# Performance work log

Hardware: AMD Instinct MI355X
Metric: run time of the kernel (lower is better)

Reference implementation:

```python
import jax, jax.numpy as jnp
import numpy as np

B, S, D, H, FF = 2, 1024, 1024, 16, 4096
EPS = 1e-6  # flax LayerNorm default


def _layernorm(x, scale, bias):
    m = jnp.mean(x, axis=-1, keepdims=True)
    v = jnp.mean(jnp.square(x - m), axis=-1, keepdims=True)
    return (x - m) * jax.lax.rsqrt(v + EPS) * scale + bias


def _attention(x, mask, w_qkv, b_qkv, w_o, b_o):
    # projection to 3*D, split into q,k,v
    p = x @ w_qkv + b_qkv                       # (B,S,3D)
    q, k, v = jnp.split(p, 3, axis=-1)          # each (B,S,D)
    hd = D // H
    # NOTE: faithful to source -- heads formed by a plain reshape of (B,S,D)
    qh = q.reshape(B, H, S, hd)
    kh = k.reshape(B, H, S, hd)
    vh = v.reshape(B, H, S, hd)
    # NOTE: scaled by sqrt(full hidden dim D), as in source (dim_key = key.shape[-1])
    scores = jnp.einsum('bhqd,bhkd->bhqk', qh, kh) / jnp.sqrt(jnp.asarray(D, x.dtype))
    scores = scores * mask                      # multiplicative mask (faithful)
    attn = jax.nn.softmax(scores, axis=-1)      # (B,H,S,S)
    ctx = jnp.einsum('bhqk,bhkd->bhqd', attn, vh).reshape(B, S, D)
    return ctx @ w_o + b_o, attn


def _geglu_ffn(x, w1, b1, wg, bg, w2, b2):
    h = x @ w1 + b1                              # (B,S,FF)
    g = h @ wg + bg                              # (B,S,2*FF)
    a, gate = g[..., :FF], g[..., FF:]
    tanh_res = jnp.tanh(gate * 0.7978845608 * (1 + 0.044715 * gate ** 2))
    act = a * 0.5 * gate * (1 + tanh_res)
    return act @ w2 + b2


def setup_inputs() -> dict:
    key = jax.random.key(0)
    ks = jax.random.split(key, 16)
    sc = 0.02
    inp = {
        'x': jax.random.normal(ks[0], (B, S, D), jnp.float32),
        'ln1_s': jnp.ones((D,), jnp.float32), 'ln1_b': jnp.zeros((D,), jnp.float32),
        'w_qkv1': jax.random.normal(ks[1], (D, 3 * D), jnp.float32) * sc,
        'b_qkv1': jnp.zeros((3 * D,), jnp.float32),
        'w_o1': jax.random.normal(ks[2], (D, D), jnp.float32) * sc,
        'b_o1': jnp.zeros((D,), jnp.float32),
        'ln2_s': jnp.ones((D,), jnp.float32), 'ln2_b': jnp.zeros((D,), jnp.float32),
        'w_qkv2': jax.random.normal(ks[3], (D, 3 * D), jnp.float32) * sc,
        'b_qkv2': jnp.zeros((3 * D,), jnp.float32),
        'w_o2': jax.random.normal(ks[4], (D, D), jnp.float32) * sc,
        'b_o2': jnp.zeros((D,), jnp.float32),
        'ln3_s': jnp.ones((D,), jnp.float32), 'ln3_b': jnp.zeros((D,), jnp.float32),
        'w1': jax.random.normal(ks[5], (D, FF), jnp.float32) * sc,
        'b1': jnp.zeros((FF,), jnp.float32),
        'wg': jax.random.normal(ks[6], (FF, 2 * FF), jnp.float32) * sc,
        'bg': jnp.zeros((2 * FF,), jnp.float32),
        'w2': jax.random.normal(ks[7], (FF, D), jnp.float32) * sc,
        'b2': jnp.zeros((D,), jnp.float32),
    }
    return inp


def reference(x, ln1_s, ln1_b, w_qkv1, b_qkv1, w_o1, b_o1,
              ln2_s, ln2_b, w_qkv2, b_qkv2, w_o2, b_o2,
              ln3_s, ln3_b, w1, b1, wg, bg, w2, b2):
    # causal mask: lower-triangular ones, multiplicative, broadcast over (B,H)
    mask = (jnp.arange(S)[:, None] >= jnp.arange(S)[None, :]).astype(jnp.int32)
    mask = jnp.broadcast_to(mask[None, None], (B, H, S, S))

    x = _layernorm(x, ln1_s, ln1_b)
    att1, attn_w1 = _attention(x, mask, w_qkv1, b_qkv1, w_o1, b_o1)
    x = x + att1                                  # dropout deterministic (identity)
    x = _layernorm(x, ln2_s, ln2_b)
    att2, attn_w2 = _attention(x, mask, w_qkv2, b_qkv2, w_o2, b_o2)
    x = x + att2
    x = _layernorm(x, ln3_s, ln3_b)
    out = _geglu_ffn(x, w1, b1, wg, bg, w2, b2)
    # NOTE: faithful to source -- final residual adds attention2 output
    x = out + att2
    return (x, attn_w1, attn_w2)
```

## Files before the change

kernel.cpp:

```cpp
#include <hip/hip_runtime.h>
#include <hip/hip_bf16.h>

#define B_ 2
#define S_ 1024
#define D_ 1024
#define H_ 16
#define HD_ 64
#define FF_ 4096
#define NROW_ (B_*S_)

typedef __hip_bfloat16 bf16;
typedef float f32x4 __attribute__((ext_vector_type(4)));
typedef int int4v __attribute__((ext_vector_type(4)));
typedef __bf16 bf16x8 __attribute__((ext_vector_type(8)));

__device__ __forceinline__ float bf2f(unsigned short u){
  return __uint_as_float((unsigned)u << 16);
}
__device__ __forceinline__ unsigned short f2bf(float f){
  unsigned u = __float_as_uint(f);
  return (unsigned short)((u + 0x7FFFu + ((u >> 16) & 1u)) >> 16);
}
__device__ __forceinline__ float gelu_gate(float a, float g){
  float t = tanhf(0.7978845608f * g * (1.f + 0.044715f * g * g));
  return a * 0.5f * g * (1.f + t);
}


__global__ __launch_bounds__(256) void tcvt(const float* __restrict__ W,
    unsigned short* __restrict__ Wt, int K, int N){
  __shared__ float tile[32][33];
  const int k0 = blockIdx.y*32, n0 = blockIdx.x*32;
  const int t = threadIdx.x;
  #pragma unroll
  for (int i = 0; i < 4; i++){
    int idx = t + i*256; int r = idx>>5, c = idx&31;
    tile[r][c] = W[(size_t)(k0+r)*N + n0 + c];
  }
  __syncthreads();
  #pragma unroll
  for (int i = 0; i < 4; i++){
    int idx = t + i*256; int r = idx>>5, c = idx&31;
    Wt[(size_t)(n0+r)*K + k0 + c] = f2bf(tile[c][r]);
  }
}

__global__ __launch_bounds__(256) void lnb_k(const float* __restrict__ x,
    const float* __restrict__ sc, const float* __restrict__ bi, unsigned short* __restrict__ y){
  const int row = blockIdx.x;
  const int t = threadIdx.x;
  const float* xr = x + (size_t)row * D_;
  float4 v = *(const float4*)&xr[t*4];
  __shared__ float red[8];
  float sum = v.x + v.y + v.z + v.w;
  #pragma unroll
  for (int o = 32; o > 0; o >>= 1) sum += __shfl_down(sum, o);
  if ((t & 63) == 0) red[t >> 6] = sum;
  __syncthreads();
  if (t == 0) red[4] = (red[0]+red[1]+red[2]+red[3]) * (1.f / D_);
  __syncthreads();
  const float mean = red[4];
  const float dx = v.x-mean, dy = v.y-mean, dz = v.z-mean, dw = v.w-mean;
  float sq = dx*dx + dy*dy + dz*dz + dw*dw;
  #pragma unroll
  for (int o = 32; o > 0; o >>= 1) sq += __shfl_down(sq, o);
  if ((t & 63) == 0) red[t >> 6] = sq;
  __syncthreads();
  if (t == 0) red[5] = (red[0]+red[1]+red[2]+red[3]) * (1.f / D_);
  __syncthreads();
  const float rstd = rsqrtf(red[5] + 1e-6f);
  float4 s4 = *(const float4*)&sc[t*4];
  float4 b4 = *(const float4*)&bi[t*4];
  ushort4 ov;
  ov.x = f2bf(dx*rstd*s4.x + b4.x);
  ov.y = f2bf(dy*rstd*s4.y + b4.y);
  ov.z = f2bf(dz*rstd*s4.z + b4.z);
  ov.w = f2bf(dw*rstd*s4.w + b4.w);
  *(ushort4*)&y[(size_t)row*D_ + t*4] = ov;
}

template<bool HAS_RES, bool RES_BF16, bool OUT_BF16>
__global__ __launch_bounds__(256) void mgemm(const unsigned short* __restrict__ A,
    const unsigned short* __restrict__ Bt, const float* __restrict__ bias,
    const void* __restrict__ res, void* __restrict__ Cv, int M, int N, int K){
  __shared__ unsigned short As[128*32];
  __shared__ unsigned short Bs[128*32];
  const int tid = threadIdx.x;
  const int bm = blockIdx.y*128, bn = blockIdx.x*128;
  const int lane = tid & 63, lq = lane >> 4, lr = lane & 15;
  const int wv = tid >> 6, wr = wv >> 1, wc = wv & 1;
  f32x4 acc[4][4] = {};
  int4v ra[2], rb[2];
  #pragma unroll
  for (int i = 0; i < 2; i++){
    int f = tid + i*256; int row = f>>2, s = f&3;
    ra[i] = *(const int4v*)&A[(size_t)(bm+row)*K + s*8];
    rb[i] = *(const int4v*)&Bt[(size_t)(bn+row)*K + s*8];
  }
  for (int k0 = 0; k0 < K; k0 += 32){
    __syncthreads();
    #pragma unroll
    for (int i = 0; i < 2; i++){
      int f = tid + i*256; int row = f>>2, s = f&3;
      int off = row*32 + ((s + (row>>1))&3)*8;
      *(int4v*)&As[off] = ra[i];
      *(int4v*)&Bs[off] = rb[i];
    }
    __syncthreads();
    if (k0 + 32 < K){
      #pragma unroll
      for (int i = 0; i < 2; i++){
        int f = tid + i*256; int row = f>>2, s = f&3;
        ra[i] = *(const int4v*)&A[(size_t)(bm+row)*K + k0+32 + s*8];
        rb[i] = *(const int4v*)&Bt[(size_t)(bn+row)*K + k0+32 + s*8];
      }
    }
    bf16x8 af[4], bfr[4];
    #pragma unroll
    for (int fm = 0; fm < 4; fm++){
      int r = wr*64 + fm*16 + lr;
      af[fm] = *(const bf16x8*)&As[r*32 + ((lq + (r>>1))&3)*8];
    }
    #pragma unroll
    for (int fn = 0; fn < 4; fn++){
      int r = wc*64 + fn*16 + lr;
      bfr[fn] = *(const bf16x8*)&Bs[r*32 + ((lq + (r>>1))&3)*8];
    }
    #pragma unroll
    for (int fm = 0; fm < 4; fm++)
      #pragma unroll
      for (int fn = 0; fn < 4; fn++)
        acc[fm][fn] = __builtin_amdgcn_mfma_f32_16x16x32_bf16(af[fm], bfr[fn], acc[fm][fn], 0, 0, 0);
  }
  #pragma unroll
  for (int fm = 0; fm < 4; fm++)
    #pragma unroll
    for (int fn = 0; fn < 4; fn++)
      #pragma unroll
      for (int rr = 0; rr < 4; rr++){
        int r = bm + wr*64 + fm*16 + lq*4 + rr;
        int c = bn + wc*64 + fn*16 + lr;
        size_t o = (size_t)r*N + c;
        float v = acc[fm][fn][rr] + bias[c];
        if (HAS_RES){
          if (RES_BF16) v += bf2f(((const unsigned short*)res)[o]);
          else          v += ((const float*)res)[o];
        }
        if (OUT_BF16) ((unsigned short*)Cv)[o] = f2bf(v);
        else          ((float*)Cv)[o] = v;
      }
}

__global__ __launch_bounds__(256) void mqkv(const unsigned short* __restrict__ A,
    const unsigned short* __restrict__ Bt, const float* __restrict__ bias,
    unsigned short* __restrict__ qh, unsigned short* __restrict__ kh, unsigned short* __restrict__ vt){
  const int K = D_;
  __shared__ unsigned short As[128*32];
  __shared__ unsigned short Bs[128*32];
  const int tid = threadIdx.x;
  const int bm = blockIdx.y*128, bn = blockIdx.x*128;
  const int lane = tid & 63, lq = lane >> 4, lr = lane & 15;
  const int wv = tid >> 6, wr = wv >> 1, wc = wv & 1;
  f32x4 acc[4][4] = {};
  int4v ra[2], rb[2];
  #pragma unroll
  for (int i = 0; i < 2; i++){
    int f = tid + i*256; int row = f>>2, s = f&3;
    ra[i] = *(const int4v*)&A[(size_t)(bm+row)*K + s*8];
    rb[i] = *(const int4v*)&Bt[(size_t)(bn+row)*K + s*8];
  }
  for (int k0 = 0; k0 < K; k0 += 32){
    __syncthreads();
    #pragma unroll
    for (int i = 0; i < 2; i++){
      int f = tid + i*256; int row = f>>2, s = f&3;
      int off = row*32 + ((s + (row>>1))&3)*8;
      *(int4v*)&As[off] = ra[i];
      *(int4v*)&Bs[off] = rb[i];
    }
    __syncthreads();
    if (k0 + 32 < K){
      #pragma unroll
      for (int i = 0; i < 2; i++){
        int f = tid + i*256; int row = f>>2, s = f&3;
        ra[i] = *(const int4v*)&A[(size_t)(bm+row)*K + k0+32 + s*8];
        rb[i] = *(const int4v*)&Bt[(size_t)(bn+row)*K + k0+32 + s*8];
      }
    }
    bf16x8 af[4], bfr[4];
    #pragma unroll
    for (int fm = 0; fm < 4; fm++){
      int r = wr*64 + fm*16 + lr;
      af[fm] = *(const bf16x8*)&As[r*32 + ((lq + (r>>1))&3)*8];
    }
    #pragma unroll
    for (int fn = 0; fn < 4; fn++){
      int r = wc*64 + fn*16 + lr;
      bfr[fn] = *(const bf16x8*)&Bs[r*32 + ((lq + (r>>1))&3)*8];
    }
    #pragma unroll
    for (int fm = 0; fm < 4; fm++)
      #pragma unroll
      for (int fn = 0; fn < 4; fn++)
        acc[fm][fn] = __builtin_amdgcn_mfma_f32_16x16x32_bf16(af[fm], bfr[fn], acc[fm][fn], 0, 0, 0);
  }
  #pragma unroll
  for (int fm = 0; fm < 4; fm++)
    #pragma unroll
    for (int fn = 0; fn < 4; fn++){
      int cbase = bn + wc*64 + fn*16 + lr;
      float bv = bias[cbase];
      if (cbase < 2*D_){
        unsigned short* dst = (cbase < D_) ? qh : kh;
        int cc = cbase & (D_-1);
        int u = cc >> 6, d2 = cc & 63;
        #pragma unroll
        for (int rr = 0; rr < 4; rr++){
          int r = bm + wr*64 + fm*16 + lq*4 + rr;
          int b = r >> 10, s = r & (S_-1);
          int h = s >> 6;
          int s2 = ((s & 63) << 4) + u;
          size_t off = (((size_t)(b*H_ + h))*S_ + s2)*HD_ + d2;
          dst[off] = f2bf(acc[fm][fn][rr] + bv);
        }
      } else {
        int cc = cbase - 2*D_;
        int u = cc >> 6, d2 = cc & 63;
        #pragma unroll
        for (int rr = 0; rr < 4; rr++){
          int r = bm + wr*64 + fm*16 + lq*4 + rr;
          int b = r >> 10, s = r & (S_-1);
          int h = s >> 6;
          int s2 = ((s & 63) << 4) + u;
          size_t off = (((size_t)(b*H_ + h))*HD_ + d2)*S_ + s2;
          vt[off] = f2bf(acc[fm][fn][rr] + bv);
        }
      }
    }
}

__global__ __launch_bounds__(256) void mgeglu(const unsigned short* __restrict__ A,
    const unsigned short* __restrict__ Wt, const float* __restrict__ bgp, unsigned short* __restrict__ act){
  const int K = FF_;
  __shared__ unsigned short As[128*32];
  __shared__ unsigned short Ba[64*32];
  __shared__ unsigned short Bg[64*32];
  const int tid = threadIdx.x;
  const int bm = blockIdx.y*128, bn = blockIdx.x*64;
  const int lane = tid & 63, lq = lane >> 4, lr = lane & 15;
  const int wv = tid >> 6, wr = wv >> 1, wc = wv & 1;
  f32x4 aa[4][2] = {};
  f32x4 ag[4][2] = {};
  int4v ra[2], rba, rbg;
  #pragma unroll
  for (int i = 0; i < 2; i++){
    int f = tid + i*256; int row = f>>2, s = f&3;
    ra[i] = *(const int4v*)&A[(size_t)(bm+row)*K + s*8];
  }
  { int row = tid>>2, s = tid&3;
    rba = *(const int4v*)&Wt[(size_t)(bn+row)*K + s*8];
    rbg = *(const int4v*)&Wt[(size_t)(FF_+bn+row)*K + s*8];
  }
  for (int k0 = 0; k0 < K; k0 += 32){
    __syncthreads();
    #pragma unroll
    for (int i = 0; i < 2; i++){
      int f = tid + i*256; int row = f>>2, s = f&3;
      *(int4v*)&As[row*32 + ((s + (row>>1))&3)*8] = ra[i];
    }
    { int row = tid>>2, s = tid&3;
      int off = row*32 + ((s + (row>>1))&3)*8;
      *(int4v*)&Ba[off] = rba;
      *(int4v*)&Bg[off] = rbg;
    }
    __syncthreads();
    if (k0 + 32 < K){
      #pragma unroll
      for (int i = 0; i < 2; i++){
        int f = tid + i*256; int row = f>>2, s = f&3;
        ra[i] = *(const int4v*)&A[(size_t)(bm+row)*K + k0+32 + s*8];
      }
      { int row = tid>>2, s = tid&3;
        rba = *(const int4v*)&Wt[(size_t)(bn+row)*K + k0+32 + s*8];
        rbg = *(const int4v*)&Wt[(size_t)(FF_+bn+row)*K + k0+32 + s*8];
      }
    }
    bf16x8 af[4], fa[2], fg[2];
    #pragma unroll
    for (int fm = 0; fm < 4; fm++){
      int r = wr*64 + fm*16 + lr;
      af[fm] = *(const bf16x8*)&As[r*32 + ((lq + (r>>1))&3)*8];
    }
    #pragma unroll
    for (int fn = 0; fn < 2; fn++){
      int r = wc*32 + fn*16 + lr;
      int off = r*32 + ((lq + (r>>1))&3)*8;
      fa[fn] = *(const bf16x8*)&Ba[off];
      fg[fn] = *(const bf16x8*)&Bg[off];
    }
    #pragma unroll
    for (int fm = 0; fm < 4; fm++)
      #pragma unroll
      for (int fn = 0; fn < 2; fn++){
        aa[fm][fn] = __builtin_amdgcn_mfma_f32_16x16x32_bf16(af[fm], fa[fn], aa[fm][fn], 0, 0, 0);
        ag[fm][fn] = __builtin_amdgcn_mfma_f32_16x16x32_bf16(af[fm], fg[fn], ag[fm][fn], 0, 0, 0);
      }
  }
  #pragma unroll
  for (int fm = 0; fm < 4; fm++)
    #pragma unroll
    for (int fn = 0; fn < 2; fn++)
      #pragma unroll
      for (int rr = 0; rr < 4; rr++){
        int r = bm + wr*64 + fm*16 + lq*4 + rr;
        int c = bn + wc*32 + fn*16 + lr;
        float a = aa[fm][fn][rr] + bgp[c];
        float g = ag[fm][fn][rr] + bgp[FF_ + c];
        act[(size_t)r*FF_ + c] = f2bf(gelu_gate(a, g));
      }
}

__global__ __launch_bounds__(256) void mscore(const unsigned short* __restrict__ qh,
    const unsigned short* __restrict__ kh, float* __restrict__ attn){
  const int kt = blockIdx.x, qt = blockIdx.y, bh = blockIdx.z;
  const int tid = threadIdx.x;
  const int lane = tid & 63, lq = lane >> 4, lr = lane & 15;
  const int wv = tid >> 6, wr = wv >> 1, wc = wv & 1;
  float* Ap = attn + (((size_t)bh*S_ + qt*128))*S_ + kt*128;

  if (kt > qt){
    #pragma unroll
    for (int i = 0; i < 16; i++){
      int f = tid + i*256;
      int r = f >> 5, c4 = f & 31;
      float4 z = {0.f,0.f,0.f,0.f};
      *(float4*)&Ap[(size_t)r*S_ + c4*4] = z;
    }
    return;
  }

  __shared__ unsigned short Qs[128*64];
  __shared__ unsigned short Ks[128*64];
  const unsigned short* Qp = qh + ((size_t)bh*S_ + qt*128)*HD_;
  const unsigned short* Kp = kh + ((size_t)bh*S_ + kt*128)*HD_;
  #pragma unroll
  for (int i = 0; i < 4; i++){
    int f = tid + i*256;
    int row = f >> 3, s = f & 7;
    int off = row*64 + ((s + row)&7)*8;
    *(int4v*)&Qs[off] = *(const int4v*)&Qp[(size_t)row*HD_ + s*8];
    *(int4v*)&Ks[off] = *(const int4v*)&Kp[(size_t)row*HD_ + s*8];
  }
  __syncthreads();
  f32x4 acc[4][4] = {};
  #pragma unroll
  for (int ks = 0; ks < 2; ks++){
    bf16x8 af[4], bfr[4];
    #pragma unroll
    for (int fm = 0; fm < 4; fm++){
      int r = wr*64 + fm*16 + lr;
      int j = ks*4 + lq;
      af[fm] = *(const bf16x8*)&Qs[r*64 + ((j + r)&7)*8];
    }
    #pragma unroll
    for (int fn = 0; fn < 4; fn++){
      int r = wc*64 + fn*16 + lr;
      int j = ks*4 + lq;
      bfr[fn] = *(const bf16x8*)&Ks[r*64 + ((j + r)&7)*8];
    }
    #pragma unroll
    for (int fm = 0; fm < 4; fm++)
      #pragma unroll
      for (int fn = 0; fn < 4; fn++)
        acc[fm][fn] = __builtin_amdgcn_mfma_f32_16x16x32_bf16(af[fm], bfr[fn], acc[fm][fn], 0, 0, 0);
  }
  const int qg0 = qt*128, kg0 = kt*128;
  #pragma unroll
  for (int fm = 0; fm < 4; fm++)
    #pragma unroll
    for (int fn = 0; fn < 4; fn++)
      #pragma unroll
      for (int rr = 0; rr < 4; rr++){
        int r = wr*64 + fm*16 + lq*4 + rr;
        int c = wc*64 + fn*16 + lr;
        float v = (kg0 + c <= qg0 + r) ? acc[fm][fn][rr] * (1.f/32.f) : 0.f;
        Ap[(size_t)r*S_ + c] = v;
      }
}

__global__ __launch_bounds__(256) void msm(float* __restrict__ attn){
  const size_t rowi = blockIdx.x;
  float* row = attn + rowi * S_;
  const int t = threadIdx.x;
  __shared__ float red[8];
  float4 v = *(const float4*)&row[t*4];
  float mx = fmaxf(fmaxf(v.x, v.y), fmaxf(v.z, v.w));
  #pragma unroll
  for (int o = 32; o > 0; o >>= 1) mx = fmaxf(mx, __shfl_down(mx, o));
  if ((t & 63) == 0) red[t >> 6] = mx;
  __syncthreads();
  if (t == 0) red[4] = fmaxf(fmaxf(red[0],red[1]), fmaxf(red[2],red[3]));
  __syncthreads();
  const float m = red[4];
  v.x = __expf(v.x - m); v.y = __expf(v.y - m);
  v.z = __expf(v.z - m); v.w = __expf(v.w - m);
  float sm = v.x + v.y + v.z + v.w;
  #pragma unroll
  for (int o = 32; o > 0; o >>= 1) sm += __shfl_down(sm, o);
  if ((t & 63) == 0) red[t >> 6] = sm;
  __syncthreads();
  if (t == 0) red[5] = red[0]+red[1]+red[2]+red[3];
  __syncthreads();
  const float inv = 1.f / red[5];
  v.x *= inv; v.y *= inv; v.z *= inv; v.w *= inv;
  *(float4*)&row[t*4] = v;
}

__global__ __launch_bounds__(256) void mctx(const float* __restrict__ attn,
    const unsigned short* __restrict__ vt, unsigned short* __restrict__ ctx){
  const int qt = blockIdx.x, bh = blockIdx.y;
  const int b = bh >> 4, h = bh & 15;
  __shared__ unsigned short As[128*32];
  __shared__ unsigned short Bs[64*32];
  const int tid = threadIdx.x;
  const int lane = tid & 63, lq = lane >> 4, lr = lane & 15;
  const int wv = tid >> 6, wr = wv >> 1, wc = wv & 1;
  const float* Ap = attn + ((size_t)bh*S_ + qt*128)*S_;
  const unsigned short* Vp = vt + (size_t)bh*HD_*S_;
  f32x4 acc[4][2] = {};
  for (int k0 = 0; k0 < S_; k0 += 32){
    __syncthreads();
    #pragma unroll
    for (int i = 0; i < 2; i++){
      int f = tid + i*256;
      int row = f >> 2, s = f & 3;
      const float* src = &Ap[(size_t)row*S_ + k0 + s*8];
      float4 v0 = *(const float4*)&src[0];
      float4 v1 = *(const float4*)&src[4];
      ushort4 u0 = {f2bf(v0.x), f2bf(v0.y), f2bf(v0.z), f2bf(v0.w)};
      ushort4 u1 = {f2bf(v1.x), f2bf(v1.y), f2bf(v1.z), f2bf(v1.w)};
      int off = row*32 + ((s + (row>>1))&3)*8;
      *(ushort4*)&As[off]   = u0;
      *(ushort4*)&As[off+4] = u1;
    }
    { int row = tid >> 2, s = tid & 3;
      int off = row*32 + ((s + (row>>1))&3)*8;
      *(int4v*)&Bs[off] = *(const int4v*)&Vp[(size_t)row*S_ + k0 + s*8];
    }
    __syncthreads();
    bf16x8 af[4], bfv[2];
    #pragma unroll
    for (int fm = 0; fm < 4; fm++){
      int r = wr*64 + fm*16 + lr;
      af[fm] = *(const bf16x8*)&As[r*32 + ((lq + (r>>1))&3)*8];
    }
    #pragma unroll
    for (int fn = 0; fn < 2; fn++){
      int r = wc*32 + fn*16 + lr;
      bfv[fn] = *(const bf16x8*)&Bs[r*32 + ((lq + (r>>1))&3)*8];
    }
    #pragma unroll
    for (int fm = 0; fm < 4; fm++)
      #pragma unroll
      for (int fn = 0; fn < 2; fn++)
        acc[fm][fn] = __builtin_amdgcn_mfma_f32_16x16x32_bf16(af[fm], bfv[fn], acc[fm][fn], 0, 0, 0);
  }
  #pragma unroll
  for (int fm = 0; fm < 4; fm++)
    #pragma unroll
    for (int fn = 0; fn < 2; fn++){
      int d = wc*32 + fn*16 + lr;
      #pragma unroll
      for (int rr = 0; rr < 4; rr++){
        int q = qt*128 + wr*64 + fm*16 + lq*4 + rr;
        size_t orow = ((size_t)b*S_ + h*HD_ + (q>>4)) * D_ + ((q&15)<<6) + d;
        ctx[orow] = f2bf(acc[fm][fn][rr]);
      }
    }
}

__global__ __launch_bounds__(256) void addbf(const unsigned short* __restrict__ a,
    const float* __restrict__ b, float* __restrict__ c){
  size_t i = ((size_t)blockIdx.x*256 + threadIdx.x)*4;
  ushort4 av = *(const ushort4*)&a[i];
  float4 bv = *(const float4*)&b[i];
  float4 o = {bf2f(av.x)+bv.x, bf2f(av.y)+bv.y, bf2f(av.z)+bv.z, bf2f(av.w)+bv.w};
  *(float4*)&c[i] = o;
}


__global__ __launch_bounds__(256) void ln_kernel(const float* __restrict__ x,
    const float* __restrict__ sc, const float* __restrict__ bi, float* __restrict__ y){
  const int row = blockIdx.x;
  const int t = threadIdx.x;
  const float* xr = x + (size_t)row * D_;
  float4 v = *(const float4*)&xr[t*4];
  __shared__ float red[8];
  float sum = v.x + v.y + v.z + v.w;
  #pragma unroll
  for (int o = 32; o > 0; o >>= 1) sum += __shfl_down(sum, o);
  if ((t & 63) == 0) red[t >> 6] = sum;
  __syncthreads();
  if (t == 0) red[4] = (red[0]+red[1]+red[2]+red[3]) * (1.f / D_);
  __syncthreads();
  const float mean = red[4];
  const float dx = v.x-mean, dy = v.y-mean, dz = v.z-mean, dw = v.w-mean;
  float sq = dx*dx + dy*dy + dz*dz + dw*dw;
  #pragma unroll
  for (int o = 32; o > 0; o >>= 1) sq += __shfl_down(sq, o);
  if ((t & 63) == 0) red[t >> 6] = sq;
  __syncthreads();
  if (t == 0) red[5] = (red[0]+red[1]+red[2]+red[3]) * (1.f / D_);
  __syncthreads();
  const float rstd = rsqrtf(red[5] + 1e-6f);
  float4 s4 = *(const float4*)&sc[t*4];
  float4 b4 = *(const float4*)&bi[t*4];
  float4 o4;
  o4.x = dx*rstd*s4.x + b4.x;
  o4.y = dy*rstd*s4.y + b4.y;
  o4.z = dz*rstd*s4.z + b4.z;
  o4.w = dw*rstd*s4.w + b4.w;
  *(float4*)&y[(size_t)row*D_ + t*4] = o4;
}

__global__ __launch_bounds__(256) void gemm_qkv_kernel(const float* __restrict__ A,
    const float* __restrict__ W, const float* __restrict__ bias,
    float* __restrict__ qh, float* __restrict__ kh, float* __restrict__ vh){
  constexpr int BK=32;
  const int K = D_, N = 3*D_;
  __shared__ float As[BK][64+4];
  __shared__ float Bs[BK][64+4];
  const int bm = blockIdx.y*64, bn = blockIdx.x*64;
  const int tid = threadIdx.x;
  const int tx = tid & 15, ty = tid >> 4;
  float acc[4][4] = {};
  for (int k0 = 0; k0 < K; k0 += BK){
    #pragma unroll
    for (int i = 0; i < 2; i++){
      int idx = tid + i*256;
      int m = idx >> 3, kq = idx & 7;
      float4 v = *(const float4*)&A[(size_t)(bm+m)*K + k0 + kq*4];
      As[kq*4+0][m] = v.x; As[kq*4+1][m] = v.y;
      As[kq*4+2][m] = v.z; As[kq*4+3][m] = v.w;
    }
    #pragma unroll
    for (int i = 0; i < 2; i++){
      int idx = tid + i*256;
      int k = idx >> 4, nq = idx & 15;
      *(float4*)&Bs[k][nq*4] = *(const float4*)&W[(size_t)(k0+k)*N + bn + nq*4];
    }
    __syncthreads();
    #pragma unroll
    for (int kk = 0; kk < BK; kk++){
      float4 a4 = *(const float4*)&As[kk][ty*4];
      float4 b4 = *(const float4*)&Bs[kk][tx*4];
      float a[4] = {a4.x,a4.y,a4.z,a4.w};
      float b[4] = {b4.x,b4.y,b4.z,b4.w};
      #pragma unroll
      for (int i = 0; i < 4; i++)
// ... 236 lines not shown
        #pragma unroll
        for (int j = 0; j < 4; j++){
          acc_a[i][j] += a[i]*pa[j];
          acc_g[i][j] += a[i]*pg[j];
        }
    }
    __syncthreads();
  }
  float4 ba4 = *(const float4*)&bgp[bn + tx*4];
  float4 bg4 = *(const float4*)&bgp[FF_ + bn + tx*4];
  const float bav[4] = {ba4.x, ba4.y, ba4.z, ba4.w};
  const float bgv[4] = {bg4.x, bg4.y, bg4.z, bg4.w};
  #pragma unroll
  for (int i = 0; i < 4; i++){
    int r = bm + ty*4 + i;
    size_t base = (size_t)r*FF_ + bn + tx*4;
    act[base+0] = f2bf(gelu_gate(acc_a[i][0]+bav[0], acc_g[i][0]+bgv[0]));
    act[base+1] = f2bf(gelu_gate(acc_a[i][1]+bav[1], acc_g[i][1]+bgv[1]));
    act[base+2] = f2bf(gelu_gate(acc_a[i][2]+bav[2], acc_g[i][2]+bgv[2]));
    act[base+3] = f2bf(gelu_gate(acc_a[i][3]+bav[3], acc_g[i][3]+bgv[3]));
  }
}

__global__ __launch_bounds__(256) void add_kernel(const float* __restrict__ a,
    const float* __restrict__ b, float* __restrict__ c){
  size_t i = ((size_t)blockIdx.x*256 + threadIdx.x)*4;
  float4 x = *(const float4*)&a[i];
  float4 y = *(const float4*)&b[i];
  float4 o = {x.x+y.x, x.y+y.y, x.z+y.z, x.w+y.w};
  *(float4*)&c[i] = o;
}


extern "C" void kernel_launch(void* const* d_in, const int* in_sizes, int n_in,
                              void* d_out, int out_size, void* d_ws, size_t ws_size,
                              hipStream_t stream){
  const float* x0     = (const float*)d_in[0];
  const float* ln1_s  = (const float*)d_in[1];
  const float* ln1_b  = (const float*)d_in[2];
  const float* w_qkv1 = (const float*)d_in[3];
  const float* b_qkv1 = (const float*)d_in[4];
  const float* w_o1   = (const float*)d_in[5];
  const float* b_o1   = (const float*)d_in[6];
  const float* ln2_s  = (const float*)d_in[7];
  const float* ln2_b  = (const float*)d_in[8];
  const float* w_qkv2 = (const float*)d_in[9];
  const float* b_qkv2 = (const float*)d_in[10];
  const float* w_o2   = (const float*)d_in[11];
  const float* b_o2   = (const float*)d_in[12];
  const float* ln3_s  = (const float*)d_in[13];
  const float* ln3_b  = (const float*)d_in[14];
  const float* w1     = (const float*)d_in[15];
  const float* b1     = (const float*)d_in[16];
  const float* wg     = (const float*)d_in[17];
  const float* bg     = (const float*)d_in[18];
  const float* w2     = (const float*)d_in[19];
  const float* b2     = (const float*)d_in[20];

  const size_t MB_ = 1u<<20;
  const size_t FAST_NEED = 148*MB_;
  float* out_x = (float*)d_out;
  float* attn1 = out_x + 2*MB_;
  float* attn2 = attn1 + 32*MB_;
  dim3 blk(256);

  if (ws_size >= FAST_NEED){
    char* w8 = (char*)d_ws;
    float* att  = (float*)(w8 + 0);
    float* xcur = (float*)(w8 + 8*MB_);
    unsigned short* lnb     = (unsigned short*)(w8 + 16*MB_);
    unsigned short* wqkv1t  = (unsigned short*)(w8 + 20*MB_);
    unsigned short* wqkv2t  = (unsigned short*)(w8 + 26*MB_);
    unsigned short* wo1t    = (unsigned short*)(w8 + 32*MB_);
    unsigned short* wo2t    = (unsigned short*)(w8 + 34*MB_);
    unsigned short* w1t     = (unsigned short*)(w8 + 36*MB_);
    unsigned short* w2t     = (unsigned short*)(w8 + 44*MB_);
    unsigned short* wgt     = (unsigned short*)(w8 + 52*MB_);
    unsigned short* qhb     = (unsigned short*)(w8 + 116*MB_);
    unsigned short* khb     = (unsigned short*)(w8 + 120*MB_);
    unsigned short* vtb     = (unsigned short*)(w8 + 124*MB_);
    unsigned short* ctxb    = (unsigned short*)(w8 + 128*MB_);
    unsigned short* hbufb   = (unsigned short*)(w8 + 116*MB_);
    unsigned short* actb    = (unsigned short*)(w8 + 132*MB_);

    tcvt<<<dim3(96,32),  blk, 0, stream>>>(w_qkv1, wqkv1t, 1024, 3072);
    tcvt<<<dim3(96,32),  blk, 0, stream>>>(w_qkv2, wqkv2t, 1024, 3072);
    tcvt<<<dim3(32,32),  blk, 0, stream>>>(w_o1,   wo1t,   1024, 1024);
    tcvt<<<dim3(32,32),  blk, 0, stream>>>(w_o2,   wo2t,   1024, 1024);
    tcvt<<<dim3(128,32), blk, 0, stream>>>(w1,     w1t,    1024, 4096);
    tcvt<<<dim3(256,128),blk, 0, stream>>>(wg,     wgt,    4096, 8192);
    tcvt<<<dim3(32,128), blk, 0, stream>>>(w2,     w2t,    4096, 1024);
    lnb_k<<<NROW_, blk, 0, stream>>>(x0, ln1_s, ln1_b, lnb);
    mqkv<<<dim3(24,16), blk, 0, stream>>>(lnb, wqkv1t, b_qkv1, qhb, khb, vtb);
    mscore<<<dim3(8,8,32), blk, 0, stream>>>(qhb, khb, attn1);
    msm<<<32768, blk, 0, stream>>>(attn1);
    mctx<<<dim3(8,32), blk, 0, stream>>>(attn1, vtb, ctxb);
    mgemm<true,true,false><<<dim3(8,16), blk, 0, stream>>>(ctxb, wo1t, b_o1, lnb, xcur, NROW_, D_, D_);
    lnb_k<<<NROW_, blk, 0, stream>>>(xcur, ln2_s, ln2_b, lnb);
    mqkv<<<dim3(24,16), blk, 0, stream>>>(lnb, wqkv2t, b_qkv2, qhb, khb, vtb);
    mscore<<<dim3(8,8,32), blk, 0, stream>>>(qhb, khb, attn2);
    msm<<<32768, blk, 0, stream>>>(attn2);
    mctx<<<dim3(8,32), blk, 0, stream>>>(attn2, vtb, ctxb);
    mgemm<false,false,false><<<dim3(8,16), blk, 0, stream>>>(ctxb, wo2t, b_o2, nullptr, att, NROW_, D_, D_);
    addbf<<<2048, blk, 0, stream>>>(lnb, att, xcur);
    lnb_k<<<NROW_, blk, 0, stream>>>(xcur, ln3_s, ln3_b, lnb);
    mgemm<false,false,true><<<dim3(32,16), blk, 0, stream>>>(lnb, w1t, b1, nullptr, hbufb, NROW_, FF_, D_);
    mgeglu<<<dim3(64,16), blk, 0, stream>>>(hbufb, wgt, bg, actb);
    mgemm<true,false,false><<<dim3(8,16), blk, 0, stream>>>(actb, w2t, b2, att, out_x, NROW_, D_, FF_);
    return;
  }

  if (ws_size < (size_t)72*MB_) return;
  float* ws = (float*)d_ws;
  const size_t M1 = 1u<<20;
  float* att    = ws;
  float* xcur   = ws + 2*M1;
  float* ln_out = ws + 4*M1;
  float* qh     = ws + 6*M1;
  float* kh     = ws + 8*M1;
  float* vh     = ws + 10*M1;
  float* ctx    = ws + 12*M1;
  float* hbuf   = ws + 6*M1;
  unsigned short* actb = (unsigned short*)(ws + 14*M1);

  ln_kernel<<<NROW_, blk, 0, stream>>>(x0, ln1_s, ln1_b, ln_out);
  gemm_qkv_kernel<<<dim3(48,32), blk, 0, stream>>>(ln_out, w_qkv1, b_qkv1, qh, kh, vh);
  attn_kernel<<<B_*H_*S_, blk, 0, stream>>>(qh, kh, attn1);
  ctx_kernel<<<dim3(16, B_*H_), blk, 0, stream>>>(attn1, vh, ctx);
  gemm_kernel<false><<<dim3(16,32), blk, 0, stream>>>(ctx, w_o1, b_o1, ln_out, xcur, NROW_, D_, D_);
  ln_kernel<<<NROW_, blk, 0, stream>>>(xcur, ln2_s, ln2_b, ln_out);
  gemm_qkv_kernel<<<dim3(48,32), blk, 0, stream>>>(ln_out, w_qkv2, b_qkv2, qh, kh, vh);
  attn_kernel<<<B_*H_*S_, blk, 0, stream>>>(qh, kh, attn2);
  ctx_kernel<<<dim3(16, B_*H_), blk, 0, stream>>>(attn2, vh, ctx);
  gemm_kernel<false><<<dim3(16,32), blk, 0, stream>>>(ctx, w_o2, b_o2, nullptr, att, NROW_, D_, D_);
  add_kernel<<<2048, blk, 0, stream>>>(ln_out, att, xcur);
  ln_kernel<<<NROW_, blk, 0, stream>>>(xcur, ln3_s, ln3_b, ln_out);
  gemm_kernel<false><<<dim3(64,32), blk, 0, stream>>>(ln_out, w1, b1, nullptr, hbuf, NROW_, FF_, D_);
  gemm_geglu_kernel<<<dim3(64,32), blk, 0, stream>>>(hbuf, wg, bg, actb);
  gemm_kernel<true><<<dim3(16,32), blk, 0, stream>>>(actb, w2, b2, att, out_x, NROW_, D_, FF_);
}
```

Before: 688.7 us.

## Load GEMM tiles directly into LDS with global_load_lds, dropping register staging

Replaces the register-staged global-to-LDS tile loads in the dense, QKV, GEGLU and ctx GEMMs with 16-byte direct global_load_lds transfers. The swizzled LDS layout is kept by permuting which global column segment each lane fetches. This cuts VGPR use and the extra LDS store instructions. It also removes the register prefetch of the next tile, so global load latency is no longer overlapped with the MFMA work of the previous tile.

```diff
diff --git a/kernel.cpp b/kernel.cpp
--- a/kernel.cpp
+++ b/kernel.cpp
@@ -24,6 +24,10 @@
 __device__ __forceinline__ float gelu_gate(float a, float g){
   float t = tanhf(0.7978845608f * g * (1.f + 0.044715f * g * g));
   return a * 0.5f * g * (1.f + t);
+}
+__device__ __forceinline__ void gll16(const void* g, void* l){
+  __builtin_amdgcn_global_load_lds((const __attribute__((address_space(1))) void*)g,
+                                   (__attribute__((address_space(3))) void*)l, 16, 0, 0);
 }
 
 
@@ -89,32 +93,19 @@
   const int bm = blockIdx.y*128, bn = blockIdx.x*128;
   const int lane = tid & 63, lq = lane >> 4, lr = lane & 15;
   const int wv = tid >> 6, wr = wv >> 1, wc = wv & 1;
+  const int j = lane & 3;
+  const int r0 = wv*32 + (lane>>2);
+  const int r1 = r0 + 16;
+  const int gs0 = (j - (r0>>1)) & 3;
+  const int gs1 = (j - (r1>>1)) & 3;
   f32x4 acc[4][4] = {};
-  int4v ra[2], rb[2];
-  #pragma unroll
-  for (int i = 0; i < 2; i++){
-    int f = tid + i*256; int row = f>>2, s = f&3;
-    ra[i] = *(const int4v*)&A[(size_t)(bm+row)*K + s*8];
-    rb[i] = *(const int4v*)&Bt[(size_t)(bn+row)*K + s*8];
-  }
   for (int k0 = 0; k0 < K; k0 += 32){
     __syncthreads();
-    #pragma unroll
-    for (int i = 0; i < 2; i++){
-      int f = tid + i*256; int row = f>>2, s = f&3;
-      int off = row*32 + ((s + (row>>1))&3)*8;
-      *(int4v*)&As[off] = ra[i];
-      *(int4v*)&Bs[off] = rb[i];
-    }
-    __syncthreads();
-    if (k0 + 32 < K){
-      #pragma unroll
-      for (int i = 0; i < 2; i++){
-        int f = tid + i*256; int row = f>>2, s = f&3;
-        ra[i] = *(const int4v*)&A[(size_t)(bm+row)*K + k0+32 + s*8];
-        rb[i] = *(const int4v*)&Bt[(size_t)(bn+row)*K + k0+32 + s*8];
-      }
-    }
+    gll16(&A [(size_t)(bm+r0)*K + k0 + gs0*8], &As[(wv*2+0)*512]);
+    gll16(&A [(size_t)(bm+r1)*K + k0 + gs1*8], &As[(wv*2+1)*512]);
+    gll16(&Bt[(size_t)(bn+r0)*K + k0 + gs0*8], &Bs[(wv*2+0)*512]);
+    gll16(&Bt[(size_t)(bn+r1)*K + k0 + gs1*8], &Bs[(wv*2+1)*512]);
+    __syncthreads();
     bf16x8 af[4], bfr[4];
     #pragma unroll
     for (int fm = 0; fm < 4; fm++){
@@ -161,32 +152,19 @@
   const int bm = blockIdx.y*128, bn = blockIdx.x*128;
   const int lane = tid & 63, lq = lane >> 4, lr = lane & 15;
   const int wv = tid >> 6, wr = wv >> 1, wc = wv & 1;
+  const int j = lane & 3;
+  const int r0 = wv*32 + (lane>>2);
+  const int r1 = r0 + 16;
+  const int gs0 = (j - (r0>>1)) & 3;
+  const int gs1 = (j - (r1>>1)) & 3;
   f32x4 acc[4][4] = {};
-  int4v ra[2], rb[2];
-  #pragma unroll
-  for (int i = 0; i < 2; i++){
-    int f = tid + i*256; int row = f>>2, s = f&3;
-    ra[i] = *(const int4v*)&A[(size_t)(bm+row)*K + s*8];
-    rb[i] = *(const int4v*)&Bt[(size_t)(bn+row)*K + s*8];
-  }
   for (int k0 = 0; k0 < K; k0 += 32){
     __syncthreads();
-    #pragma unroll
-    for (int i = 0; i < 2; i++){
-      int f = tid + i*256; int row = f>>2, s = f&3;
-      int off = row*32 + ((s + (row>>1))&3)*8;
-      *(int4v*)&As[off] = ra[i];
-      *(int4v*)&Bs[off] = rb[i];
-    }
-    __syncthreads();
-    if (k0 + 32 < K){
-      #pragma unroll
-      for (int i = 0; i < 2; i++){
-        int f = tid + i*256; int row = f>>2, s = f&3;
-        ra[i] = *(const int4v*)&A[(size_t)(bm+row)*K + k0+32 + s*8];
-        rb[i] = *(const int4v*)&Bt[(size_t)(bn+row)*K + k0+32 + s*8];
-      }
-    }
+    gll16(&A [(size_t)(bm+r0)*K + k0 + gs0*8], &As[(wv*2+0)*512]);
+    gll16(&A [(size_t)(bm+r1)*K + k0 + gs1*8], &As[(wv*2+1)*512]);
+    gll16(&Bt[(size_t)(bn+r0)*K + k0 + gs0*8], &Bs[(wv*2+0)*512]);
+    gll16(&Bt[(size_t)(bn+r1)*K + k0 + gs1*8], &Bs[(wv*2+1)*512]);
+    __syncthreads();
     bf16x8 af[4], bfr[4];
     #pragma unroll
     for (int fm = 0; fm < 4; fm++){
@@ -249,42 +227,22 @@
   const int bm = blockIdx.y*128, bn = blockIdx.x*64;
   const int lane = tid & 63, lq = lane >> 4, lr = lane & 15;
   const int wv = tid >> 6, wr = wv >> 1, wc = wv & 1;
+  const int j = lane & 3;
+  const int r0 = wv*32 + (lane>>2);
+  const int r1 = r0 + 16;
+  const int gs0 = (j - (r0>>1)) & 3;
+  const int gs1 = (j - (r1>>1)) & 3;
+  const int rB = wv*16 + (lane>>2);
+  const int gsB = (j - (rB>>1)) & 3;
   f32x4 aa[4][2] = {};
   f32x4 ag[4][2] = {};
-  int4v ra[2], rba, rbg;
-  #pragma unroll
-  for (int i = 0; i < 2; i++){
-    int f = tid + i*256; int row = f>>2, s = f&3;
-    ra[i] = *(const int4v*)&A[(size_t)(bm+row)*K + s*8];
-  }
-  { int row = tid>>2, s = tid&3;
-    rba = *(const int4v*)&Wt[(size_t)(bn+row)*K + s*8];
-    rbg = *(const int4v*)&Wt[(size_t)(FF_+bn+row)*K + s*8];
-  }
   for (int k0 = 0; k0 < K; k0 += 32){
     __syncthreads();
-    #pragma unroll
-    for (int i = 0; i < 2; i++){
-      int f = tid + i*256; int row = f>>2, s = f&3;
-      *(int4v*)&As[row*32 + ((s + (row>>1))&3)*8] = ra[i];
-    }
-    { int row = tid>>2, s = tid&3;
-      int off = row*32 + ((s + (row>>1))&3)*8;
-      *(int4v*)&Ba[off] = rba;
-      *(int4v*)&Bg[off] = rbg;
-    }
-    __syncthreads();
-    if (k0 + 32 < K){
-      #pragma unroll
-      for (int i = 0; i < 2; i++){
-        int f = tid + i*256; int row = f>>2, s = f&3;
-        ra[i] = *(const int4v*)&A[(size_t)(bm+row)*K + k0+32 + s*8];
-      }
-      { int row = tid>>2, s = tid&3;
-        rba = *(const int4v*)&Wt[(size_t)(bn+row)*K + k0+32 + s*8];
-        rbg = *(const int4v*)&Wt[(size_t)(FF_+bn+row)*K + k0+32 + s*8];
-      }
-    }
+    gll16(&A [(size_t)(bm+r0)*K + k0 + gs0*8], &As[(wv*2+0)*512]);
+    gll16(&A [(size_t)(bm+r1)*K + k0 + gs1*8], &As[(wv*2+1)*512]);
+    gll16(&Wt[(size_t)(bn+rB)*K      + k0 + gsB*8], &Ba[wv*512]);
+    gll16(&Wt[(size_t)(FF_+bn+rB)*K  + k0 + gsB*8], &Bg[wv*512]);
+    __syncthreads();
     bf16x8 af[4], fa[2], fg[2];
     #pragma unroll
     for (int fm = 0; fm < 4; fm++){
@@ -359,14 +317,14 @@
     #pragma unroll
     for (int fm = 0; fm < 4; fm++){
       int r = wr*64 + fm*16 + lr;
-      int j = ks*4 + lq;
-      af[fm] = *(const bf16x8*)&Qs[r*64 + ((j + r)&7)*8];
+      int jj = ks*4 + lq;
+      af[fm] = *(const bf16x8*)&Qs[r*64 + ((jj + r)&7)*8];
     }
     #pragma unroll
     for (int fn = 0; fn < 4; fn++){
       int r = wc*64 + fn*16 + lr;
-      int j = ks*4 + lq;
-      bfr[fn] = *(const bf16x8*)&Ks[r*64 + ((j + r)&7)*8];
+      int jj = ks*4 + lq;
+      bfr[fn] = *(const bf16x8*)&Ks[r*64 + ((jj + r)&7)*8];
     }
     #pragma unroll
     for (int fm = 0; fm < 4; fm++)
@@ -427,9 +385,13 @@
   const int wv = tid >> 6, wr = wv >> 1, wc = wv & 1;
   const float* Ap = attn + ((size_t)bh*S_ + qt*128)*S_;
   const unsigned short* Vp = vt + (size_t)bh*HD_*S_;
+  const int j = lane & 3;
+  const int rB = wv*16 + (lane>>2);
+  const int gsB = (j - (rB>>1)) & 3;
   f32x4 acc[4][2] = {};
   for (int k0 = 0; k0 < S_; k0 += 32){
     __syncthreads();
+    gll16(&Vp[(size_t)rB*S_ + k0 + gsB*8], &Bs[wv*512]);
     #pragma unroll
     for (int i = 0; i < 2; i++){
       int f = tid + i*256;
@@ -442,10 +404,6 @@
       int off = row*32 + ((s + (row>>1))&3)*8;
       *(ushort4*)&As[off]   = u0;
       *(ushort4*)&As[off+4] = u1;
-    }
-    { int row = tid >> 2, s = tid & 3;
-      int off = row*32 + ((s + (row>>1))&3)*8;
-      *(int4v*)&Bs[off] = *(const int4v*)&Vp[(size_t)row*S_ + k0 + s*8];
     }
     __syncthreads();
     bf16x8 af[4], bfv[2];
```

After: 760.6 us. +10.4%, slower.

## Fuse attention score, softmax and PV into two-pass stats plus recompute kernels

Applied to the files above, without the earlier changes.

Replaces the score-write, row-softmax and context kernels with a two-pass flash-style scheme. The first kernel computes per-row max and sum with an online softmax, and analytically accounts for the masked zeros in the upper tiles. The second kernel recomputes QK^T, writes the normalized probabilities once, and accumulates P·V from shared memory. This removes the fp32 attention-matrix round trips (write, read-modify-write, read), at the cost of computing QK^T twice. The second kernel also uses a larger shared-memory footprint, which may lower occupancy.

```diff
diff --git a/kernel.cpp b/kernel.cpp
--- a/kernel.cpp
+++ b/kernel.cpp
@@ -320,150 +320,232 @@
       }
 }
 
-__global__ __launch_bounds__(256) void mscore(const unsigned short* __restrict__ qh,
-    const unsigned short* __restrict__ kh, float* __restrict__ attn){
-  const int kt = blockIdx.x, qt = blockIdx.y, bh = blockIdx.z;
+__global__ __launch_bounds__(256) void mstats(const unsigned short* __restrict__ qh,
+    const unsigned short* __restrict__ kh, float2* __restrict__ stats){
+  const int qt = blockIdx.x, bh = blockIdx.y;
   const int tid = threadIdx.x;
   const int lane = tid & 63, lq = lane >> 4, lr = lane & 15;
   const int wv = tid >> 6, wr = wv >> 1, wc = wv & 1;
-  float* Ap = attn + (((size_t)bh*S_ + qt*128))*S_ + kt*128;
-
-  if (kt > qt){
-    #pragma unroll
-    for (int i = 0; i < 16; i++){
-      int f = tid + i*256;
-      int r = f >> 5, c4 = f & 31;
-      float4 z = {0.f,0.f,0.f,0.f};
-      *(float4*)&Ap[(size_t)r*S_ + c4*4] = z;
-    }
-    return;
-  }
-
   __shared__ unsigned short Qs[128*64];
   __shared__ unsigned short Ks[128*64];
+  __shared__ float2 st[2][2][64];
   const unsigned short* Qp = qh + ((size_t)bh*S_ + qt*128)*HD_;
-  const unsigned short* Kp = kh + ((size_t)bh*S_ + kt*128)*HD_;
   #pragma unroll
   for (int i = 0; i < 4; i++){
     int f = tid + i*256;
     int row = f >> 3, s = f & 7;
-    int off = row*64 + ((s + row)&7)*8;
-    *(int4v*)&Qs[off] = *(const int4v*)&Qp[(size_t)row*HD_ + s*8];
-    *(int4v*)&Ks[off] = *(const int4v*)&Kp[(size_t)row*HD_ + s*8];
-  }
-  __syncthreads();
-  f32x4 acc[4][4] = {};
-  #pragma unroll
-  for (int ks = 0; ks < 2; ks++){
-    bf16x8 af[4], bfr[4];
-    #pragma unroll
-    for (int fm = 0; fm < 4; fm++){
-      int r = wr*64 + fm*16 + lr;
-      int j = ks*4 + lq;
-      af[fm] = *(const bf16x8*)&Qs[r*64 + ((j + r)&7)*8];
-    }
-    #pragma unroll
-    for (int fn = 0; fn < 4; fn++){
-      int r = wc*64 + fn*16 + lr;
-      int j = ks*4 + lq;
-      bfr[fn] = *(const bf16x8*)&Ks[r*64 + ((j + r)&7)*8];
-    }
+    *(int4v*)&Qs[row*64 + ((s + row)&7)*8] = *(const int4v*)&Qp[(size_t)row*HD_ + s*8];
+  }
+  float m[4][4], l[4][4];
+  #pragma unroll
+  for (int fm = 0; fm < 4; fm++)
+    #pragma unroll
+    for (int rr = 0; rr < 4; rr++){ m[fm][rr] = -3.4e38f; l[fm][rr] = 0.f; }
+  const int qg0 = qt*128;
+  for (int kt = 0; kt <= qt; kt++){
+    __syncthreads();
+    const unsigned short* Kp = kh + ((size_t)bh*S_ + kt*128)*HD_;
+    #pragma unroll
+    for (int i = 0; i < 4; i++){
+      int f = tid + i*256;
+      int row = f >> 3, s = f & 7;
+      *(int4v*)&Ks[row*64 + ((s + row)&7)*8] = *(const int4v*)&Kp[(size_t)row*HD_ + s*8];
+    }
+    __syncthreads();
+    f32x4 acc[4][4] = {};
+    #pragma unroll
+    for (int ks = 0; ks < 2; ks++){
+      bf16x8 af[4], bfr[4];
+      #pragma unroll
+      for (int fm = 0; fm < 4; fm++){
+        int r = wr*64 + fm*16 + lr;
+        af[fm] = *(const bf16x8*)&Qs[r*64 + ((ks*4+lq + r)&7)*8];
+      }
+      #pragma unroll
+      for (int fn = 0; fn < 4; fn++){
+        int r = wc*64 + fn*16 + lr;
+        bfr[fn] = *(const bf16x8*)&Ks[r*64 + ((ks*4+lq + r)&7)*8];
+      }
+      #pragma unroll
+      for (int fm = 0; fm < 4; fm++)
+        #pragma unroll
+        for (int fn = 0; fn < 4; fn++)
+          acc[fm][fn] = __builtin_amdgcn_mfma_f32_16x16x32_bf16(af[fm], bfr[fn], acc[fm][fn], 0, 0, 0);
+    }
+    const int kg0 = kt*128;
     #pragma unroll
     for (int fm = 0; fm < 4; fm++)
-      #pragma unroll
-      for (int fn = 0; fn < 4; fn++)
-        acc[fm][fn] = __builtin_amdgcn_mfma_f32_16x16x32_bf16(af[fm], bfr[fn], acc[fm][fn], 0, 0, 0);
-  }
-  const int qg0 = qt*128, kg0 = kt*128;
-  #pragma unroll
-  for (int fm = 0; fm < 4; fm++)
-    #pragma unroll
-    for (int fn = 0; fn < 4; fn++)
       #pragma unroll
       for (int rr = 0; rr < 4; rr++){
         int r = wr*64 + fm*16 + lq*4 + rr;
-        int c = wc*64 + fn*16 + lr;
-        float v = (kg0 + c <= qg0 + r) ? acc[fm][fn][rr] * (1.f/32.f) : 0.f;
-        Ap[(size_t)r*S_ + c] = v;
-      }
-}
-
-__global__ __launch_bounds__(256) void msm(float* __restrict__ attn){
-  const size_t rowi = blockIdx.x;
-  float* row = attn + rowi * S_;
-  const int t = threadIdx.x;
-  __shared__ float red[8];
-  float4 v = *(const float4*)&row[t*4];
-  float mx = fmaxf(fmaxf(v.x, v.y), fmaxf(v.z, v.w));
-  #pragma unroll
-  for (int o = 32; o > 0; o >>= 1) mx = fmaxf(mx, __shfl_down(mx, o));
-  if ((t & 63) == 0) red[t >> 6] = mx;
-  __syncthreads();
-  if (t == 0) red[4] = fmaxf(fmaxf(red[0],red[1]), fmaxf(red[2],red[3]));
-  __syncthreads();
-  const float m = red[4];
-  v.x = __expf(v.x - m); v.y = __expf(v.y - m);
-  v.z = __expf(v.z - m); v.w = __expf(v.w - m);
-  float sm = v.x + v.y + v.z + v.w;
-  #pragma unroll
-  for (int o = 32; o > 0; o >>= 1) sm += __shfl_down(sm, o);
-  if ((t & 63) == 0) red[t >> 6] = sm;
-  __syncthreads();
-  if (t == 0) red[5] = red[0]+red[1]+red[2]+red[3];
-  __syncthreads();
-  const float inv = 1.f / red[5];
-  v.x *= inv; v.y *= inv; v.z *= inv; v.w *= inv;
-  *(float4*)&row[t*4] = v;
-}
-
-__global__ __launch_bounds__(256) void mctx(const float* __restrict__ attn,
-    const unsigned short* __restrict__ vt, unsigned short* __restrict__ ctx){
+        float v0 = (kg0 + wc*64 +  0 + lr <= qg0 + r) ? acc[fm][0][rr]*(1.f/32.f) : 0.f;
+        float v1 = (kg0 + wc*64 + 16 + lr <= qg0 + r) ? acc[fm][1][rr]*(1.f/32.f) : 0.f;
+        float v2 = (kg0 + wc*64 + 32 + lr <= qg0 + r) ? acc[fm][2][rr]*(1.f/32.f) : 0.f;
+        float v3 = (kg0 + wc*64 + 48 + lr <= qg0 + r) ? acc[fm][3][rr]*(1.f/32.f) : 0.f;
+        float tmax = fmaxf(fmaxf(v0,v1), fmaxf(v2,v3));
+        tmax = fmaxf(tmax, __shfl_xor(tmax,1));
+        tmax = fmaxf(tmax, __shfl_xor(tmax,2));
+        tmax = fmaxf(tmax, __shfl_xor(tmax,4));
+        tmax = fmaxf(tmax, __shfl_xor(tmax,8));
+        float mn = fmaxf(m[fm][rr], tmax);
+        float se = __expf(v0-mn)+__expf(v1-mn)+__expf(v2-mn)+__expf(v3-mn);
+        se += __shfl_xor(se,1); se += __shfl_xor(se,2);
+        se += __shfl_xor(se,4); se += __shfl_xor(se,8);
+        l[fm][rr] = l[fm][rr]*__expf(m[fm][rr]-mn) + se;
+        m[fm][rr] = mn;
+      }
+  }
+  if (lr == 0){
+    #pragma unroll
+    for (int fm = 0; fm < 4; fm++)
+      #pragma unroll
+      for (int rr = 0; rr < 4; rr++){
+        float2 v; v.x = m[fm][rr]; v.y = l[fm][rr];
+        st[wr][wc][fm*16 + lq*4 + rr] = v;
+      }
+  }
+  __syncthreads();
+  if (wc == 0 && lr == 0){
+    const float nz = (float)((7 - qt)*128);
+    #pragma unroll
+    for (int fm = 0; fm < 4; fm++)
+      #pragma unroll
+      for (int rr = 0; rr < 4; rr++){
+        int r64 = fm*16 + lq*4 + rr;
+        float2 a = st[wr][0][r64], b = st[wr][1][r64];
+        float mf = fmaxf(a.x, b.x);
+        float lf = a.y*__expf(a.x-mf) + b.y*__expf(b.x-mf);
+        if (nz > 0.f){
+          float mz = fmaxf(mf, 0.f);
+          lf = lf*__expf(mf-mz) + nz*__expf(-mz);
+          mf = mz;
+        }
+        float2 o; o.x = mf; o.y = lf;
+        stats[(size_t)bh*S_ + qt*128 + wr*64 + r64] = o;
+      }
+  }
+}
+
+__global__ __launch_bounds__(256) void mpv(const unsigned short* __restrict__ qh,
+    const unsigned short* __restrict__ kh, const unsigned short* __restrict__ vt,
+    const float2* __restrict__ stats, float* __restrict__ attn, unsigned short* __restrict__ ctx){
   const int qt = blockIdx.x, bh = blockIdx.y;
   const int b = bh >> 4, h = bh & 15;
-  __shared__ unsigned short As[128*32];
-  __shared__ unsigned short Bs[64*32];
   const int tid = threadIdx.x;
   const int lane = tid & 63, lq = lane >> 4, lr = lane & 15;
   const int wv = tid >> 6, wr = wv >> 1, wc = wv & 1;
-  const float* Ap = attn + ((size_t)bh*S_ + qt*128)*S_;
+  __shared__ unsigned short Qs[128*64];
+  __shared__ unsigned short Ks[128*64];
+  __shared__ unsigned short Pt[128*128];
+  __shared__ unsigned short Vt[64*128];
+  const unsigned short* Qp = qh + ((size_t)bh*S_ + qt*128)*HD_;
   const unsigned short* Vp = vt + (size_t)bh*HD_*S_;
-  f32x4 acc[4][2] = {};
-  for (int k0 = 0; k0 < S_; k0 += 32){
-    __syncthreads();
-    #pragma unroll
-    for (int i = 0; i < 2; i++){
+  float* Ap = attn + ((size_t)bh*S_ + qt*128)*S_;
+  #pragma unroll
+  for (int i = 0; i < 4; i++){
+    int f = tid + i*256;
+    int row = f >> 3, s = f & 7;
+    *(int4v*)&Qs[row*64 + ((s + row)&7)*8] = *(const int4v*)&Qp[(size_t)row*HD_ + s*8];
+  }
+  float mS[4][4], lI[4][4];
+  #pragma unroll
+  for (int fm = 0; fm < 4; fm++)
+    #pragma unroll
+    for (int rr = 0; rr < 4; rr++){
+      float2 s2 = stats[(size_t)bh*S_ + qt*128 + wr*64 + fm*16 + lq*4 + rr];
+      mS[fm][rr] = s2.x; lI[fm][rr] = 1.f / s2.y;
+    }
+  const int qg0 = qt*128;
+  f32x4 oacc[4][2] = {};
+  for (int kt = 0; kt < 8; kt++){
+    __syncthreads();
+    #pragma unroll
+    for (int i = 0; i < 4; i++){
       int f = tid + i*256;
-      int row = f >> 2, s = f & 3;
-      const float* src = &Ap[(size_t)row*S_ + k0 + s*8];
-      float4 v0 = *(const float4*)&src[0];
-      float4 v1 = *(const float4*)&src[4];
-      ushort4 u0 = {f2bf(v0.x), f2bf(v0.y), f2bf(v0.z), f2bf(v0.w)};
-      ushort4 u1 = {f2bf(v1.x), f2bf(v1.y), f2bf(v1.z), f2bf(v1.w)};
-      int off = row*32 + ((s + (row>>1))&3)*8;
-      *(ushort4*)&As[off]   = u0;
-      *(ushort4*)&As[off+4] = u1;
-    }
-    { int row = tid >> 2, s = tid & 3;
-      int off = row*32 + ((s + (row>>1))&3)*8;
-      *(int4v*)&Bs[off] = *(const int4v*)&Vp[(size_t)row*S_ + k0 + s*8];
-    }
-    __syncthreads();
-    bf16x8 af[4], bfv[2];
-    #pragma unroll
-    for (int fm = 0; fm < 4; fm++){
-      int r = wr*64 + fm*16 + lr;
-      af[fm] = *(const bf16x8*)&As[r*32 + ((lq + (r>>1))&3)*8];
-    }
-    #pragma unroll
-    for (int fn = 0; fn < 2; fn++){
-      int r = wc*32 + fn*16 + lr;
-      bfv[fn] = *(const bf16x8*)&Bs[r*32 + ((lq + (r>>1))&3)*8];
-    }
-    #pragma unroll
-    for (int fm = 0; fm < 4; fm++)
-      #pragma unroll
-      for (int fn = 0; fn < 2; fn++)
-        acc[fm][fn] = __builtin_amdgcn_mfma_f32_16x16x32_bf16(af[fm], bfv[fn], acc[fm][fn], 0, 0, 0);
+      int row = f >> 4, s = f & 15;
+      *(int4v*)&Vt[row*128 + ((s + row)&15)*8] = *(const int4v*)&Vp[(size_t)row*S_ + kt*128 + s*8];
+    }
+    if (kt <= qt){
+      const unsigned short* Kp = kh + ((size_t)bh*S_ + kt*128)*HD_;
+      #pragma unroll
+      for (int i = 0; i < 4; i++){
+        int f = tid + i*256;
+        int row = f >> 3, s = f & 7;
+        *(int4v*)&Ks[row*64 + ((s + row)&7)*8] = *(const int4v*)&Kp[(size_t)row*HD_ + s*8];
+      }
+      __syncthreads();
+      f32x4 acc[4][4] = {};
+      #pragma unroll
+      for (int ks = 0; ks < 2; ks++){
+        bf16x8 af[4], bfr[4];
+        #pragma unroll
+        for (int fm = 0; fm < 4; fm++){
+          int r = wr*64 + fm*16 + lr;
+          af[fm] = *(const bf16x8*)&Qs[r*64 + ((ks*4+lq + r)&7)*8];
+        }
+        #pragma unroll
+        for (int fn = 0; fn < 4; fn++){
+          int r = wc*64 + fn*16 + lr;
+          bfr[fn] = *(const bf16x8*)&Ks[r*64 + ((ks*4+lq + r)&7)*8];
+        }
+        #pragma unroll
+        for (int fm = 0; fm < 4; fm++)
+          #pragma unroll
+          for (int fn = 0; fn < 4; fn++)
+            acc[fm][fn] = __builtin_amdgcn_mfma_f32_16x16x32_bf16(af[fm], bfr[fn], acc[fm][fn], 0, 0, 0);
+      }
+      const int kg0 = kt*128;
+      #pragma unroll
+      for (int fm = 0; fm < 4; fm++)
+        #pragma unroll
+        for (int fn = 0; fn < 4; fn++)
+          #pragma unroll
+          for (int rr = 0; rr < 4; rr++){
+            int r = wr*64 + fm*16 + lq*4 + rr;
+            int c = wc*64 + fn*16 + lr;
+            float v = (kg0 + c <= qg0 + r) ? acc[fm][fn][rr]*(1.f/32.f) : 0.f;
+            float p = __expf(v - mS[fm][rr]) * lI[fm][rr];
+            Ap[(size_t)r*S_ + kg0 + c] = p;
+            Pt[r*128 + (((c>>3) + r)&15)*8 + (c&7)] = f2bf(p);
+          }
+      __syncthreads();
+    } else {
+      __syncthreads();
+      int rt = tid >> 1, hk = tid & 1;
+      float2 srow = stats[(size_t)bh*S_ + qt*128 + rt];
+      float p = __expf(-srow.x) * (1.f / srow.y);
+      unsigned short pb = f2bf(p);
+      int rep = (unsigned)pb | ((unsigned)pb << 16);
+      int4v pv = {rep, rep, rep, rep};
+      float4 pf = {p, p, p, p};
+      #pragma unroll
+      for (int sl = 0; sl < 8; sl++){
+        int slot = hk*8 + sl;
+        *(int4v*)&Pt[rt*128 + ((slot + rt)&15)*8] = pv;
+        *(float4*)&Ap[(size_t)rt*S_ + kt*128 + hk*64 + sl*8] = pf;
+        *(float4*)&Ap[(size_t)rt*S_ + kt*128 + hk*64 + sl*8 + 4] = pf;
+      }
+      __syncthreads();
+    }
+    #pragma unroll
+    for (int ks = 0; ks < 4; ks++){
+      bf16x8 af[4], bfv[2];
+      #pragma unroll
+      for (int fm = 0; fm < 4; fm++){
+        int r = wr*64 + fm*16 + lr;
+        af[fm] = *(const bf16x8*)&Pt[r*128 + ((ks*4+lq + r)&15)*8];
+      }
+      #pragma unroll
+      for (int fn = 0; fn < 2; fn++){
+        int r = wc*32 + fn*16 + lr;
+        bfv[fn] = *(const bf16x8*)&Vt[r*128 + ((ks*4+lq + r)&15)*8];
+      }
+      #pragma unroll
+      for (int fm = 0; fm < 4; fm++)
+        #pragma unroll
+        for (int fn = 0; fn < 2; fn++)
+          oacc[fm][fn] = __builtin_amdgcn_mfma_f32_16x16x32_bf16(af[fm], bfv[fn], oacc[fm][fn], 0, 0, 0);
+    }
   }
   #pragma unroll
   for (int fm = 0; fm < 4; fm++)
@@ -474,7 +556,7 @@
       for (int rr = 0; rr < 4; rr++){
         int q = qt*128 + wr*64 + fm*16 + lq*4 + rr;
         size_t orow = ((size_t)b*S_ + h*HD_ + (q>>4)) * D_ + ((q&15)<<6) + d;
-        ctx[orow] = f2bf(acc[fm][fn][rr]);
+        ctx[orow] = f2bf(oacc[fm][fn][rr]);
       }
     }
 }
@@ -877,6 +959,7 @@
     unsigned short* ctxb    = (unsigned short*)(w8 + 128*MB_);
     unsigned short* hbufb   = (unsigned short*)(w8 + 116*MB_);
     unsigned short* actb    = (unsigned short*)(w8 + 132*MB_);
+    float2* stats           = (float2*)(w8 + 132*MB_);
 
     tcvt<<<dim3(96,32),  blk, 0, stream>>>(w_qkv1, wqkv1t, 1024, 3072);
     tcvt<<<dim3(96,32),  blk, 0, stream>>>(w_qkv2, wqkv2t, 1024, 3072);
@@ -887,15 +970,13 @@
     tcvt<<<dim3(32,128), blk, 0, stream>>>(w2,     w2t,    4096, 1024);
     lnb_k<<<NROW_, blk, 0, stream>>>(x0, ln1_s, ln1_b, lnb);
     mqkv<<<dim3(24,16), blk, 0, stream>>>(lnb, wqkv1t, b_qkv1, qhb, khb, vtb);
-    mscore<<<dim3(8,8,32), blk, 0, stream>>>(qhb, khb, attn1);
-    msm<<<32768, blk, 0, stream>>>(attn1);
-    mctx<<<dim3(8,32), blk, 0, stream>>>(attn1, vtb, ctxb);
+    mstats<<<dim3(8,32), blk, 0, stream>>>(qhb, khb, stats);
+    mpv<<<dim3(8,32), blk, 0, stream>>>(qhb, khb, vtb, stats, attn1, ctxb);
     mgemm<true,true,false><<<dim3(8,16), blk, 0, stream>>>(ctxb, wo1t, b_o1, lnb, xcur, NROW_, D_, D_);
     lnb_k<<<NROW_, blk, 0, stream>>>(xcur, ln2_s, ln2_b, lnb);
     mqkv<<<dim3(24,16), blk, 0, stream>>>(lnb, wqkv2t, b_qkv2, qhb, khb, vtb);
-    mscore<<<dim3(8,8,32), blk, 0, stream>>>(qhb, khb, attn2);
-    msm<<<32768, blk, 0, stream>>>(attn2);
-    mctx<<<dim3(8,32), blk, 0, stream>>>(attn2, vtb, ctxb);
+    mstats<<<dim3(8,32), blk, 0, stream>>>(qhb, khb, stats);
+    mpv<<<dim3(8,32), blk, 0, stream>>>(qhb, khb, vtb, stats, attn2, ctxb);
     mgemm<false,false,false><<<dim3(8,16), blk, 0, stream>>>(ctxb, wo2t, b_o2, nullptr, att, NROW_, D_, D_);
     addbf<<<2048, blk, 0, stream>>>(lnb, att, xcur);
     lnb_k<<<NROW_, blk, 0, stream>>>(xcur, ln3_s, ln3_b, lnb);
```

New measurement: 669.9 us. -2.7%, faster.
